# Optimization experiments

Hardware: AMD Instinct MI355X
Metric: run time of the kernel (lower is better)

The kernel has to match this reference:

```python
import math
import jax, jax.numpy as jnp
import numpy as np

L, D, H, F, V, S = 4, 1024, 16, 4096, 50257, 2048
HS = D // H
EPS = 1e-5
STD = 0.02


def setup_inputs() -> dict:
    key = jax.random.key(0)
    keys = iter(jax.random.split(key, 24))

    def rn(shape):
        return (jax.random.normal(next(keys), shape, jnp.float32) * STD)

    inp = {
        "input_ids": jax.random.randint(next(keys), (1, S), 0, V, dtype=jnp.int64),
        "tok_emb": rn((V, D)),
        "pos_emb": rn((S, D)),
        # per-layer stacked params; linear weights stored [in, out]
        "Wq": rn((L, D, D)), "bq": jnp.zeros((L, D)),
        "Wk": rn((L, D, D)), "bk": jnp.zeros((L, D)),
        "Wv": rn((L, D, D)), "bv": jnp.zeros((L, D)),
        "Wo": rn((L, D, D)), "bo": jnp.zeros((L, D)),
        "W1": rn((L, D, F)), "b1": jnp.zeros((L, F)),
        "W2": rn((L, F, D)), "b2": jnp.zeros((L, D)),
        "ln1w": jnp.ones((L, D)), "ln1b": jnp.zeros((L, D)),
        "ln2w": jnp.ones((L, D)), "ln2b": jnp.zeros((L, D)),
        "lnfw": jnp.ones((D,)), "lnfb": jnp.zeros((D,)),
        "lm_head": rn((V, D)),  # torch Linear weight layout [out, in]
    }
    return inp


def _layernorm(x, w, b):
    m = jnp.mean(x, axis=-1, keepdims=True)
    v = jnp.mean(jnp.square(x - m), axis=-1, keepdims=True)
    return (x - m) * jax.lax.rsqrt(v + EPS) * w + b


def reference(input_ids, tok_emb, pos_emb, Wq, bq, Wk, bk, Wv, bv, Wo, bo,
              W1, b1, W2, b2, ln1w, ln1b, ln2w, ln2b, lnfw, lnfb, lm_head):
    B, Sq = input_ids.shape
    h = tok_emb[input_ids] + pos_emb[None, :Sq]  # [B,S,D]
    causal = jnp.tril(jnp.ones((Sq, Sq), dtype=bool))
    scale = 1.0 / math.sqrt(HS)

    def block(h, p):
        wq, bq_, wk, bk_, wv, bv_, wo, bo_, w1, b1_, w2, b2_, l1w, l1b, l2w, l2b = p
        x = _layernorm(h, l1w, l1b)
        q = (x @ wq + bq_).reshape(B, Sq, H, HS).transpose(0, 2, 1, 3)
        k = (x @ wk + bk_).reshape(B, Sq, H, HS).transpose(0, 2, 1, 3)
        v = (x @ wv + bv_).reshape(B, Sq, H, HS).transpose(0, 2, 1, 3)
        scores = jnp.einsum('bhqd,bhkd->bhqk', q, k) * scale
        scores = jnp.where(causal, scores, jnp.finfo(scores.dtype).min)
        attn = jax.nn.softmax(scores, axis=-1)  # dropout is identity at eval
        out = jnp.einsum('bhqk,bhkd->bhqd', attn, v)
        out = out.transpose(0, 2, 1, 3).reshape(B, Sq, D)
        h = h + out @ wo + bo_
        x = _layernorm(h, l2w, l2b)
        h = h + jax.nn.gelu(x @ w1 + b1_, approximate=False) @ w2 + b2_
        return h, None

    h, _ = jax.lax.scan(block, h, (Wq, bq, Wk, bk, Wv, bv, Wo, bo,
                                   W1, b1, W2, b2, ln1w, ln1b, ln2w, ln2b))
    h = _layernorm(h, lnfw, lnfb)
    logits = h @ lm_head.T  # [B,S,V]
    return logits
```

## Files before the change

kernel.cpp:

```cpp
#include <hip/hip_runtime.h>
#include <math.h>
#include <stdint.h>


#define SEQ 2048
#define DIM 1024
#define NHEAD 16
#define FFN 4096
#define VOCAB 50257
#define NLAYER 4
#define LNEPS 1e-5f
#define QKVD 3072
#define KVB 128

using bf16x8 = __attribute__((ext_vector_type(8))) short;
using s16x4  = __attribute__((ext_vector_type(4))) short;
using f32x4  = __attribute__((ext_vector_type(4))) float;
using fl4    = __attribute__((ext_vector_type(4))) float;

static __device__ __forceinline__ short f2bf(float f) {
  uint32_t u = __float_as_uint(f);
  u = (u + 0x7fffu + ((u >> 16) & 1u)) >> 16;
  return (short)u;
}
static __device__ __forceinline__ float bf2f(short s) {
  return __uint_as_float(((uint32_t)(uint16_t)s) << 16);
}
static __device__ __forceinline__ void gload_lds16(const void* g, void* l) {
  __builtin_amdgcn_global_load_lds((const __attribute__((address_space(1))) void*)g,
                                   (__attribute__((address_space(3))) void*)l, 16, 0, 0);
}

__global__ void embed_kernel(const int* __restrict__ ids,
                             const float* __restrict__ tok,
                             const float* __restrict__ pos,
                             float* __restrict__ h) {
  int i = blockIdx.x * blockDim.x + threadIdx.x;
  if (i < SEQ * DIM) {
    int s = i / DIM, d = i % DIM;
    h[i] = tok[(long)ids[s] * DIM + d] + pos[i];
  }
}

__global__ void ln_kernel(const float* __restrict__ x, const float* __restrict__ w,
                          const float* __restrict__ b, short* __restrict__ y) {
  int row = blockIdx.x;
  const float* xr = x + (long)row * DIM;
  short* yr = y + (long)row * DIM;
  int tid = threadIdx.x;
  float v0 = xr[tid], v1 = xr[tid + 256], v2 = xr[tid + 512], v3 = xr[tid + 768];
  __shared__ float red[8];
  float s = v0 + v1 + v2 + v3;
#pragma unroll
  for (int o = 32; o >= 1; o >>= 1) s += __shfl_xor(s, o);
  if ((tid & 63) == 0) red[tid >> 6] = s;
  __syncthreads();
  float mean = (red[0] + red[1] + red[2] + red[3]) * (1.f / DIM);
  float d0 = v0 - mean, d1 = v1 - mean, d2 = v2 - mean, d3 = v3 - mean;
  float q = d0 * d0 + d1 * d1 + d2 * d2 + d3 * d3;
#pragma unroll
  for (int o = 32; o >= 1; o >>= 1) q += __shfl_xor(q, o);
  if ((tid & 63) == 0) red[4 + (tid >> 6)] = q;
  __syncthreads();
  float var = (red[4] + red[5] + red[6] + red[7]) * (1.f / DIM);
  float rstd = rsqrtf(var + LNEPS);
  yr[tid]       = f2bf(d0 * rstd * w[tid] + b[tid]);
  yr[tid + 256] = f2bf(d1 * rstd * w[tid + 256] + b[tid + 256]);
  yr[tid + 512] = f2bf(d2 * rstd * w[tid + 512] + b[tid + 512]);
  yr[tid + 768] = f2bf(d3 * rstd * w[tid + 768] + b[tid + 768]);
}

__global__ void transpose_w(const float* __restrict__ in, short* __restrict__ out,
                            int K, int N) {
  __shared__ float t[32][33];
  int c0 = blockIdx.x * 32, r0 = blockIdx.y * 32;
  int tx = threadIdx.x & 31, ty = threadIdx.x >> 5;
#pragma unroll
  for (int i = 0; i < 4; i++)
    t[ty + i * 8][tx] = in[(long)(r0 + ty + i * 8) * N + c0 + tx];
  __syncthreads();
#pragma unroll
  for (int i = 0; i < 4; i++)
    out[(long)(c0 + ty + i * 8) * K + r0 + tx] = f2bf(t[tx][ty + i * 8]);
}

struct TW4 { const float* src[4]; short* dst[4]; };
__global__ void transpose_w4(TW4 p) {
  const float* in = p.src[blockIdx.z];
  short* out = p.dst[blockIdx.z];
  __shared__ float t[32][33];
  int c0 = blockIdx.x * 32, r0 = blockIdx.y * 32;
  int tx = threadIdx.x & 31, ty = threadIdx.x >> 5;
#pragma unroll
  for (int i = 0; i < 4; i++)
    t[ty + i * 8][tx] = in[(long)(r0 + ty + i * 8) * DIM + c0 + tx];
  __syncthreads();
#pragma unroll
  for (int i = 0; i < 4; i++)
    out[(long)(c0 + ty + i * 8) * DIM + r0 + tx] = f2bf(t[tx][ty + i * 8]);
}

__global__ void transpose_v(const short* __restrict__ qkv, short* __restrict__ vt) {
  __shared__ short t[64][72];
  int s0 = blockIdx.x * 64, c0 = blockIdx.y * 64;
  int tid = threadIdx.x;
#pragma unroll
  for (int i = 0; i < 2; i++) {
    int ca = i * 256 + tid;
    int row = ca >> 3, cp = ca & 7;
    bf16x8 v = *(const bf16x8*)(qkv + (long)(s0 + row) * QKVD + 2 * DIM + c0 + cp * 8);
    *(bf16x8*)&t[row][cp * 8] = v;
  }
  __syncthreads();
#pragma unroll
  for (int i = 0; i < 2; i++) {
    int ca = i * 256 + tid;
    int crow = ca >> 3, sp = ca & 7;
    s16x4 a, b;
#pragma unroll
    for (int u = 0; u < 4; u++) a[u] = t[sp * 8 + u][crow];
#pragma unroll
    for (int u = 0; u < 4; u++) b[u] = t[sp * 8 + 4 + u][crow];
    bf16x8 o;
#pragma unroll
    for (int u = 0; u < 4; u++) { o[u] = a[u]; o[4 + u] = b[u]; }
    *(bf16x8*)(vt + (long)(c0 + crow) * SEQ + s0 + sp * 8) = o;
  }
}

__global__ void conv_bf16(const float* __restrict__ in, short* __restrict__ out, long n4) {
  long i = (long)blockIdx.x * blockDim.x + threadIdx.x;
  long stride = (long)gridDim.x * blockDim.x;
  for (; i < n4; i += stride) {
    fl4 v = *(const fl4*)(in + i * 4);
    s16x4 o;
    o[0] = f2bf(v[0]); o[1] = f2bf(v[1]); o[2] = f2bf(v[2]); o[3] = f2bf(v[3]);
    *(s16x4*)(out + i * 4) = o;
  }
}

__global__ void bias_cat(const float* __restrict__ bq, const float* __restrict__ bk,
                         const float* __restrict__ bv, float* __restrict__ out) {
  int i = blockIdx.x * 256 + threadIdx.x;
  if (i < QKVD) out[i] = i < DIM ? bq[i] : (i < 2 * DIM ? bk[i - DIM] : bv[i - 2 * DIM]);
}

template <bool GELU, bool RES, bool BIAS, bool OUTBF16, int KS, bool XCDSWZ>
__global__ __launch_bounds__(512) void gemm8(
    const short* __restrict__ A, const short* __restrict__ Bt,
    const float* __restrict__ bias, const float* __restrict__ res,
    void* __restrict__ Cout, int N, int Kfull) {
  __shared__ short lds[3][(256 + 128) * 64];
  const int tid = threadIdx.x, wid = tid >> 6, lane = tid & 63;
  const int l16 = lane & 15, lg = lane >> 4;
  int bx = blockIdx.x, by = blockIdx.y;
  if (XCDSWZ) {
    int gx = gridDim.x, nwg = gx * gridDim.y;
    int flat = by * gx + bx;
    int nf = (flat & 7) * (nwg >> 3) + (flat >> 3);
    bx = nf % gx; by = nf / gx;
  }
  const long m0 = (long)bx * 256, n0 = (long)by * 128;
  const int K = Kfull / KS;
  const int kbase = blockIdx.z * K;
  const int NT = K / 64;
  const int wr = (wid >> 1) * 64, wc = (wid & 1) * 64;

#define STAGE8(t, b)                                                            \
  {                                                                             \
    short* As_ = lds[b];                                                        \
    short* Bs_ = lds[b] + 256 * 64;                                             \
    int kk_ = kbase + (t) * 64;                                                 \
    _Pragma("unroll")                                                           \
    for (int i_ = 0; i_ < 4; i_++) {                                            \
      int ca_ = i_ * 512 + tid;                                                 \
      int row_ = ca_ >> 3, cp_ = ca_ & 7, c_ = cp_ ^ (row_ & 7);                \
      gload_lds16(A + (m0 + row_) * (long)Kfull + kk_ + c_ * 8,                 \
                  As_ + (i_ * 512 + wid * 64) * 8);                             \
    }                                                                           \
    _Pragma("unroll")                                                           \
    for (int i_ = 0; i_ < 2; i_++) {                                            \
      int ca_ = i_ * 512 + tid;                                                 \
      int row_ = ca_ >> 3, cp_ = ca_ & 7, c_ = cp_ ^ (row_ & 7);                \
      int rowb_ = (int)n0 + row_;                                               \
      if (rowb_ > N - 1) rowb_ = N - 1;                                         \
      gload_lds16(Bt + (long)rowb_ * Kfull + kk_ + c_ * 8,                      \
                  Bs_ + (i_ * 512 + wid * 64) * 8);                             \
    }                                                                           \
  }

  f32x4 acc[4][4] = {};
  STAGE8(0, 0);
  STAGE8(1, 1);
  asm volatile("s_waitcnt vmcnt(6)" ::: "memory");
  __builtin_amdgcn_s_barrier();
  __builtin_amdgcn_sched_barrier(0);

  for (int t = 0; t < NT; t++) {
    const int b = t % 3;
    if (t + 2 < NT) STAGE8(t + 2, (t + 2) % 3);
    const short* As = lds[b];
    const short* Bs = lds[b] + 256 * 64;
    bf16x8 af[4][2], bfr[4][2];
#pragma unroll
    for (int m = 0; m < 4; m++) {
      int row = wr + m * 16 + l16;
#pragma unroll
      for (int ks = 0; ks < 2; ks++)
        af[m][ks] = *(const bf16x8*)((const char*)As + row * 128 + (((ks * 4 + lg) ^ (row & 7)) * 16));
    }
#pragma unroll
    for (int n = 0; n < 4; n++) {
      int row = wc + n * 16 + l16;
#pragma unroll
      for (int ks = 0; ks < 2; ks++)
        bfr[n][ks] = *(const bf16x8*)((const char*)Bs + row * 128 + (((ks * 4 + lg) ^ (row & 7)) * 16));
    }
    __builtin_amdgcn_s_setprio(1);
#pragma unroll
    for (int ks = 0; ks < 2; ks++)
#pragma unroll
      for (int m = 0; m < 4; m++)
#pragma unroll
        for (int n = 0; n < 4; n++)
          acc[m][n] = __builtin_amdgcn_mfma_f32_16x16x32_bf16(af[m][ks], bfr[n][ks], acc[m][n], 0, 0, 0);
    __builtin_amdgcn_s_setprio(0);
    if (t + 2 < NT) {
      asm volatile("s_waitcnt vmcnt(6)" ::: "memory");
    } else if (t + 1 < NT) {
      asm volatile("s_waitcnt vmcnt(0)" ::: "memory");
    }
    if (t + 1 < NT) {
      __builtin_amdgcn_s_barrier();
      __builtin_amdgcn_sched_barrier(0);
    }
  }
#undef STAGE8

  const int lr4 = lg * 4;
  if (KS == 1) {
#pragma unroll
    for (int m = 0; m < 4; m++)
#pragma unroll
      for (int n = 0; n < 4; n++)
#pragma unroll
        for (int r = 0; r < 4; r++) {
          long row = m0 + wr + m * 16 + lr4 + r;
          long col = n0 + wc + n * 16 + l16;
          if (col < N) {
            float v = acc[m][n][r];
            if (BIAS) v += bias[col];
            if (GELU) v = 0.5f * v * (1.f + erff(v * 0.70710678118f));
            if (RES) v += res[row * (long)N + col];
            if (OUTBF16) ((short*)Cout)[row * (long)N + col] = f2bf(v);
            else ((float*)Cout)[row * (long)N + col] = v;
          }
        }
  } else {
    long M = (long)gridDim.x * 256;
    float* P = (float*)Cout + (long)blockIdx.z * M * N;
#pragma unroll
    for (int m = 0; m < 4; m++)
#pragma unroll
      for (int n = 0; n < 4; n++)
#pragma unroll
        for (int r = 0; r < 4; r++) {
          long row = m0 + wr + m * 16 + lr4 + r;
          long col = n0 + wc + n * 16 + l16;
          P[row * (long)N + col] = acc[m][n][r];
        }
  }
}

template <int KS>
__global__ void reduce_k(const float* __restrict__ part, const float* __restrict__ bias,
                         float* __restrict__ h, int N, long MN) {
  long i = ((long)blockIdx.x * 256 + threadIdx.x) * 4;
  if (i >= MN) return;
  fl4 s = *(const fl4*)(h + i);
  fl4 b = *(const fl4*)(bias + (int)(i % N));
  s[0] += b[0]; s[1] += b[1]; s[2] += b[2]; s[3] += b[3];
#pragma unroll
  for (int ks = 0; ks < KS; ks++) {
    fl4 p = *(const fl4*)(part + (long)ks * MN + i);
    s[0] += p[0]; s[1] += p[1]; s[2] += p[2]; s[3] += p[3];
  }
  *(fl4*)(h + i) = s;
}

__global__ __launch_bounds__(256) void attn_mfma(const short* __restrict__ qkv,
                                                 const short* __restrict__ vtg,
                                                 short* __restrict__ Oa) {
  int hh = blockIdx.x, qb = blockIdx.y;
  int q0 = qb * 64;
  int tid = threadIdx.x, wv = tid >> 6, lane = tid & 63;
  int l16 = lane & 15, lg = lane >> 4;
  int hcol = hh * 64;
  __shared__ short Ks[KVB * 64];
  __shared__ short Vt[64 * KVB];
  __shared__ short Pl[4][16 * KVB];

  bf16x8 qf[2];
  {
    const short* qrow = qkv + (long)(q0 + wv * 16 + l16) * QKVD + hcol;
#pragma unroll
    for (int dc = 0; dc < 2; dc++) {
      bf16x8 t = *(const bf16x8*)(qrow + dc * 32 + lg * 8);
#pragma unroll
      for (int j = 0; j < 8; j++) t[j] = f2bf(bf2f(t[j]) * 0.125f);
      qf[dc] = t;
    }
  }
  f32x4 of[4] = {};
  float mrun[4], lrun[4];
#pragma unroll
  for (int r = 0; r < 4; r++) { mrun[r] = -3e38f; lrun[r] = 0.f; }

  int nt = qb / 2 + 1;
  for (int kt = 0; kt < nt; kt++) {
    int k0 = kt * KVB;
    __syncthreads();
#pragma unroll
    for (int i = 0; i < 4; i++) {
      int ca = i * 256 + tid;
      int row = ca >> 3, cp = ca & 7, c = cp ^ (row & 7);
      int ldsoff = (i * 256 + wv * 64) * 8;
      gload_lds16(qkv + (long)(k0 + row) * QKVD + DIM + hcol + c * 8, (short*)Ks + ldsoff);
    }
#pragma unroll
    for (int i = 0; i < 4; i++) {
      int ca = i * 256 + tid;
      int row = ca >> 4, cp = ca & 15, c = cp ^ (row & 7);
      int ldsoff = (i * 256 + wv * 64) * 8;
      gload_lds16(vtg + (long)(hcol + row) * SEQ + k0 + c * 8, (short*)Vt + ldsoff);
    }
    __syncthreads();

    f32x4 sacc[8] = {};
#pragma unroll
    for (int kc = 0; kc < 8; kc++) {
      int row = kc * 16 + l16;
#pragma unroll
      for (int dc = 0; dc < 2; dc++) {
        bf16x8 kf = *(const bf16x8*)((const char*)Ks + row * 128 + (((dc * 4 + lg) ^ (row & 7)) * 16));
        sacc[kc] = __builtin_amdgcn_mfma_f32_16x16x32_bf16(qf[dc], kf, sacc[kc], 0, 0, 0);
      }
    }

    float sv[8][4], pf[8][4];
#pragma unroll
    for (int kc = 0; kc < 8; kc++)
#pragma unroll
      for (int r = 0; r < 4; r++) sv[kc][r] = sacc[kc][r];
    if (kt == nt - 1) {
#pragma unroll
      for (int kc = 0; kc < 8; kc++)
#pragma unroll
        for (int r = 0; r < 4; r++) {
          int kg = k0 + kc * 16 + l16;
          int rg = q0 + wv * 16 + lg * 4 + r;
          if (kg > rg) sv[kc][r] = -3e38f;
        }
    }
    float corr[4];
#pragma unroll
    for (int r = 0; r < 4; r++) {
      float m01 = fmaxf(sv[0][r], sv[1][r]), m23 = fmaxf(sv[2][r], sv[3][r]);
      float m45 = fmaxf(sv[4][r], sv[5][r]), m67 = fmaxf(sv[6][r], sv[7][r]);
      float mt = fmaxf(fmaxf(m01, m23), fmaxf(m45, m67));
#pragma unroll
      for (int o = 8; o >= 1; o >>= 1) mt = fmaxf(mt, __shfl_xor(mt, o));
      float mn = fmaxf(mrun[r], mt);
      corr[r] = __expf(mrun[r] - mn);
      mrun[r] = mn;
      float ps = 0.f;
#pragma unroll
      for (int kc = 0; kc < 8; kc++) {
        float p = __expf(sv[kc][r] - mn);
        pf[kc][r] = p;
        ps += p;
      }
#pragma unroll
      for (int o = 8; o >= 1; o >>= 1) ps += __shfl_xor(ps, o);
      lrun[r] = lrun[r] * corr[r] + ps;
    }
#pragma unroll
    for (int c = 0; c < 4; c++)
#pragma unroll
      for (int r = 0; r < 4; r++) of[c][r] *= corr[r];
#pragma unroll
    for (int kc = 0; kc < 8; kc++)
#pragma unroll
      for (int r = 0; r < 4; r++) {
        int row = lg * 4 + r, col = kc * 16 + l16;
        int chunk = col >> 3;
        *(short*)((char*)Pl[wv] + row * 256 + ((chunk ^ (row & 7)) * 16) + (col & 7) * 2) = f2bf(pf[kc][r]);
      }
    bf16x8 pfr[4];
#pragma unroll
    for (int kc2 = 0; kc2 < 4; kc2++) {
      int cl = kc2 * 4 + lg;
      pfr[kc2] = *(const bf16x8*)((const char*)Pl[wv] + l16 * 256 + ((cl ^ (l16 & 7)) * 16));
    }
#pragma unroll
    for (int c = 0; c < 4; c++)
#pragma unroll
      for (int kc2 = 0; kc2 < 4; kc2++) {
        int vrow = c * 16 + l16;
        int cl = kc2 * 4 + lg;
        bf16x8 vf = *(const bf16x8*)((const char*)Vt + vrow * 256 + ((cl ^ (vrow & 7)) * 16));
        of[c] = __builtin_amdgcn_mfma_f32_16x16x32_bf16(pfr[kc2], vf, of[c], 0, 0, 0);
      }
  }
#pragma unroll
  for (int c = 0; c < 4; c++)
#pragma unroll
    for (int r = 0; r < 4; r++) {
      int rowg = q0 + wv * 16 + lg * 4 + r;
      int colg = hcol + c * 16 + l16;
      Oa[(long)rowg * DIM + colg] = f2bf(of[c][r] / lrun[r]);
    }
}

extern "C" void kernel_launch(void* const* d_in, const int* in_sizes, int n_in,
                              void* d_out, int out_size, void* d_ws, size_t ws_size,
                              hipStream_t stream) {
  const int* ids = (const int*)d_in[0];
  const float* tok = (const float*)d_in[1];
  const float* pos = (const float*)d_in[2];
  const float* Wq = (const float*)d_in[3];
  const float* bq = (const float*)d_in[4];
  const float* Wk = (const float*)d_in[5];
  const float* bk = (const float*)d_in[6];
  const float* Wv = (const float*)d_in[7];
  const float* bv = (const float*)d_in[8];
  const float* Wo = (const float*)d_in[9];
  const float* bo = (const float*)d_in[10];
  const float* W1 = (const float*)d_in[11];
  const float* b1 = (const float*)d_in[12];
  const float* W2 = (const float*)d_in[13];
  const float* b2 = (const float*)d_in[14];
  const float* ln1w = (const float*)d_in[15];
  const float* ln1b = (const float*)d_in[16];
  const float* ln2w = (const float*)d_in[17];
  const float* ln2b = (const float*)d_in[18];
  const float* lnfw = (const float*)d_in[19];
  const float* lnfb = (const float*)d_in[20];
  const float* lmh = (const float*)d_in[21];
  float* out = (float*)d_out;

  char* wsb = (char*)d_ws;
  float* h = (float*)wsb;
  short* x = (short*)(wsb + 8388608);
  char* big = wsb + 8388608 + 4194304;
  short* qkv  = (short*)big;
  short* a    = (short*)(big + 12582912);
  short* vt   = (short*)(big + 16777216);
  short* fbuf = (short*)(big + 20971520);
  float* pproj = (float*)fbuf;
  float* pffn2 = (float*)big;
  char* wdyn = big + 37748736;
  short* wqkvT = (short*)wdyn;
  short* woT   = (short*)(wdyn + 6291456);
  short* w1T   = (short*)(wdyn + 8388608);
  short* w2T   = (short*)(wdyn + 16777216);
  float* bias3 = (float*)(wdyn + 25165824);
  short* lmhB = (short*)big;

  const long MN = (long)SEQ * DIM;

  embed_kernel<<<(SEQ * DIM + 255) / 256, 256, 0, stream>>>(ids, tok, pos, h);

  dim3 gQKV(SEQ / 256, QKVD / 128);
  dim3 gPROJ(SEQ / 256, DIM / 128, 2);
  dim3 gFFN1(SEQ / 256, FFN / 128);
  dim3 gFFN2(SEQ / 256, DIM / 128, 2);
  dim3 gV(SEQ / 256, (VOCAB + 127) / 128);

  for (int l = 0; l < NLAYER; l++) {
    TW4 tw;
    tw.src[0] = Wq + (long)l * DIM * DIM; tw.dst[0] = wqkvT;
    tw.src[1] = Wk + (long)l * DIM * DIM; tw.dst[1] = wqkvT + (long)DIM * DIM;
    tw.src[2] = Wv + (long)l * DIM * DIM; tw.dst[2] = wqkvT + (long)2 * DIM * DIM;
    tw.src[3] = Wo + (long)l * DIM * DIM; tw.dst[3] = woT;
    transpose_w4<<<dim3(32, 32, 4), 256, 0, stream>>>(tw);
    transpose_w<<<dim3(128, 32), 256, 0, stream>>>(W1 + (long)l * DIM * FFN, w1T, DIM, FFN);
    transpose_w<<<dim3(32, 128), 256, 0, stream>>>(W2 + (long)l * FFN * DIM, w2T, FFN, DIM);
    bias_cat<<<12, 256, 0, stream>>>(bq + (long)l * DIM, bk + (long)l * DIM, bv + (long)l * DIM, bias3);

    ln_kernel<<<SEQ, 256, 0, stream>>>(h, ln1w + (long)l * DIM, ln1b + (long)l * DIM, x);
    gemm8<false, false, true, true, 1, true><<<gQKV, 512, 0, stream>>>(x, wqkvT, bias3, nullptr, qkv, QKVD, DIM);
    transpose_v<<<dim3(SEQ / 64, DIM / 64), 256, 0, stream>>>(qkv, vt);
    attn_mfma<<<dim3(NHEAD, SEQ / 64), 256, 0, stream>>>(qkv, vt, a);
    gemm8<false, false, false, false, 2, true><<<gPROJ, 512, 0, stream>>>(a, woT, nullptr, nullptr, pproj, DIM, DIM);
    reduce_k<2><<<(int)(MN / 1024), 256, 0, stream>>>(pproj, bo + (long)l * DIM, h, DIM, MN);
    ln_kernel<<<SEQ, 256, 0, stream>>>(h, ln2w + (long)l * DIM, ln2b + (long)l * DIM, x);
    gemm8<true, false, true, true, 1, true><<<gFFN1, 512, 0, stream>>>(x, w1T, b1 + (long)l * FFN, nullptr, fbuf, FFN, DIM);
    gemm8<false, false, false, false, 2, true><<<gFFN2, 512, 0, stream>>>(fbuf, w2T, nullptr, nullptr, pffn2, DIM, FFN);
    reduce_k<2><<<(int)(MN / 1024), 256, 0, stream>>>(pffn2, b2 + (long)l * DIM, h, DIM, MN);
  }

  ln_kernel<<<SEQ, 256, 0, stream>>>(h, lnfw, lnfb, x);
  conv_bf16<<<2048, 256, 0, stream>>>(lmh, lmhB, (long)VOCAB * DIM / 4);
  gemm8<false, false, false, false, 1, true><<<gV, 512, 0, stream>>>(x, lmhB, nullptr, nullptr, out, VOCAB, DIM);
}
```

Before: 1.145 ms.

## Replace 256x128x64 GEMM tile with 128x128x32 tile, 4 waves, 3 blocks per CU

Swaps the 8-wave GEMM kernel (256x128 output tile, K-step 64) for a 4-wave version with a 128x128 tile and K-step 32, changing the LDS swizzle to match the 64-byte rows. The smaller LDS footprint and launch_bounds(256,3) let more workgroups share each CU, and grids double along M so more blocks are available for the many GEMMs. In exchange, each block reuses its data less, more K iterations with barriers are needed, and each sync covers fewer MFMAs.

```diff
diff --git a/kernel.cpp b/kernel.cpp
--- a/kernel.cpp
+++ b/kernel.cpp
@@ -146,11 +146,11 @@
 }
 
 template <bool GELU, bool RES, bool BIAS, bool OUTBF16, int KS, bool XCDSWZ>
-__global__ __launch_bounds__(512) void gemm8(
+__global__ __launch_bounds__(256, 3) void gemm4(
     const short* __restrict__ A, const short* __restrict__ Bt,
     const float* __restrict__ bias, const float* __restrict__ res,
     void* __restrict__ Cout, int N, int Kfull) {
-  __shared__ short lds[3][(256 + 128) * 64];
+  __shared__ short lds[3][(128 + 128) * 32];
   const int tid = threadIdx.x, wid = tid >> 6, lane = tid & 63;
   const int l16 = lane & 15, lg = lane >> 4;
   int bx = blockIdx.x, by = blockIdx.y;
@@ -160,73 +160,67 @@
     int nf = (flat & 7) * (nwg >> 3) + (flat >> 3);
     bx = nf % gx; by = nf / gx;
   }
-  const long m0 = (long)bx * 256, n0 = (long)by * 128;
+  const long m0 = (long)bx * 128, n0 = (long)by * 128;
   const int K = Kfull / KS;
   const int kbase = blockIdx.z * K;
-  const int NT = K / 64;
+  const int NT = K / 32;
   const int wr = (wid >> 1) * 64, wc = (wid & 1) * 64;
 
-#define STAGE8(t, b)                                                            \
+#define STAGE4(t, b)                                                            \
   {                                                                             \
     short* As_ = lds[b];                                                        \
-    short* Bs_ = lds[b] + 256 * 64;                                             \
-    int kk_ = kbase + (t) * 64;                                                 \
+    short* Bs_ = lds[b] + 128 * 32;                                             \
+    int kk_ = kbase + (t) * 32;                                                 \
     _Pragma("unroll")                                                           \
-    for (int i_ = 0; i_ < 4; i_++) {                                            \
-      int ca_ = i_ * 512 + tid;                                                 \
-      int row_ = ca_ >> 3, cp_ = ca_ & 7, c_ = cp_ ^ (row_ & 7);                \
+    for (int i_ = 0; i_ < 2; i_++) {                                            \
+      int ca_ = i_ * 256 + tid;                                                 \
+      int row_ = ca_ >> 2, cp_ = ca_ & 3, c_ = cp_ ^ ((row_ >> 1) & 3);         \
       gload_lds16(A + (m0 + row_) * (long)Kfull + kk_ + c_ * 8,                 \
-                  As_ + (i_ * 512 + wid * 64) * 8);                             \
+                  As_ + (i_ * 256 + wid * 64) * 8);                             \
     }                                                                           \
     _Pragma("unroll")                                                           \
     for (int i_ = 0; i_ < 2; i_++) {                                            \
-      int ca_ = i_ * 512 + tid;                                                 \
-      int row_ = ca_ >> 3, cp_ = ca_ & 7, c_ = cp_ ^ (row_ & 7);                \
+      int ca_ = i_ * 256 + tid;                                                 \
+      int row_ = ca_ >> 2, cp_ = ca_ & 3, c_ = cp_ ^ ((row_ >> 1) & 3);         \
       int rowb_ = (int)n0 + row_;                                               \
       if (rowb_ > N - 1) rowb_ = N - 1;                                         \
       gload_lds16(Bt + (long)rowb_ * Kfull + kk_ + c_ * 8,                      \
-                  Bs_ + (i_ * 512 + wid * 64) * 8);                             \
+                  Bs_ + (i_ * 256 + wid * 64) * 8);                             \
     }                                                                           \
   }
 
   f32x4 acc[4][4] = {};
-  STAGE8(0, 0);
-  STAGE8(1, 1);
-  asm volatile("s_waitcnt vmcnt(6)" ::: "memory");
+  STAGE4(0, 0);
+  STAGE4(1, 1);
+  asm volatile("s_waitcnt vmcnt(4)" ::: "memory");
   __builtin_amdgcn_s_barrier();
   __builtin_amdgcn_sched_barrier(0);
 
   for (int t = 0; t < NT; t++) {
     const int b = t % 3;
-    if (t + 2 < NT) STAGE8(t + 2, (t + 2) % 3);
+    if (t + 2 < NT) STAGE4(t + 2, (t + 2) % 3);
     const short* As = lds[b];
-    const short* Bs = lds[b] + 256 * 64;
-    bf16x8 af[4][2], bfr[4][2];
+    const short* Bs = lds[b] + 128 * 32;
+    bf16x8 af[4], bfr[4];
 #pragma unroll
     for (int m = 0; m < 4; m++) {
       int row = wr + m * 16 + l16;
-#pragma unroll
-      for (int ks = 0; ks < 2; ks++)
-        af[m][ks] = *(const bf16x8*)((const char*)As + row * 128 + (((ks * 4 + lg) ^ (row & 7)) * 16));
+      af[m] = *(const bf16x8*)((const char*)As + row * 64 + ((lg ^ ((row >> 1) & 3)) * 16));
     }
 #pragma unroll
     for (int n = 0; n < 4; n++) {
       int row = wc + n * 16 + l16;
-#pragma unroll
-      for (int ks = 0; ks < 2; ks++)
-        bfr[n][ks] = *(const bf16x8*)((const char*)Bs + row * 128 + (((ks * 4 + lg) ^ (row & 7)) * 16));
+      bfr[n] = *(const bf16x8*)((const char*)Bs + row * 64 + ((lg ^ ((row >> 1) & 3)) * 16));
     }
     __builtin_amdgcn_s_setprio(1);
 #pragma unroll
-    for (int ks = 0; ks < 2; ks++)
-#pragma unroll
-      for (int m = 0; m < 4; m++)
-#pragma unroll
-        for (int n = 0; n < 4; n++)
-          acc[m][n] = __builtin_amdgcn_mfma_f32_16x16x32_bf16(af[m][ks], bfr[n][ks], acc[m][n], 0, 0, 0);
+    for (int m = 0; m < 4; m++)
+#pragma unroll
+      for (int n = 0; n < 4; n++)
+        acc[m][n] = __builtin_amdgcn_mfma_f32_16x16x32_bf16(af[m], bfr[n], acc[m][n], 0, 0, 0);
     __builtin_amdgcn_s_setprio(0);
     if (t + 2 < NT) {
-      asm volatile("s_waitcnt vmcnt(6)" ::: "memory");
+      asm volatile("s_waitcnt vmcnt(4)" ::: "memory");
     } else if (t + 1 < NT) {
       asm volatile("s_waitcnt vmcnt(0)" ::: "memory");
     }
@@ -235,7 +229,7 @@
       __builtin_amdgcn_sched_barrier(0);
     }
   }
-#undef STAGE8
+#undef STAGE4
 
   const int lr4 = lg * 4;
   if (KS == 1) {
@@ -257,7 +251,7 @@
           }
         }
   } else {
-    long M = (long)gridDim.x * 256;
+    long M = (long)gridDim.x * 128;
     float* P = (float*)Cout + (long)blockIdx.z * M * N;
 #pragma unroll
     for (int m = 0; m < 4; m++)
@@ -471,11 +465,11 @@
 
   embed_kernel<<<(SEQ * DIM + 255) / 256, 256, 0, stream>>>(ids, tok, pos, h);
 
-  dim3 gQKV(SEQ / 256, QKVD / 128);
-  dim3 gPROJ(SEQ / 256, DIM / 128, 2);
-  dim3 gFFN1(SEQ / 256, FFN / 128);
-  dim3 gFFN2(SEQ / 256, DIM / 128, 2);
-  dim3 gV(SEQ / 256, (VOCAB + 127) / 128);
+  dim3 gQKV(SEQ / 128, QKVD / 128);
+  dim3 gPROJ(SEQ / 128, DIM / 128, 2);
+  dim3 gFFN1(SEQ / 128, FFN / 128);
+  dim3 gFFN2(SEQ / 128, DIM / 128, 2);
+  dim3 gV(SEQ / 128, (VOCAB + 127) / 128);
 
   for (int l = 0; l < NLAYER; l++) {
     TW4 tw;
@@ -489,18 +483,18 @@
     bias_cat<<<12, 256, 0, stream>>>(bq + (long)l * DIM, bk + (long)l * DIM, bv + (long)l * DIM, bias3);
 
     ln_kernel<<<SEQ, 256, 0, stream>>>(h, ln1w + (long)l * DIM, ln1b + (long)l * DIM, x);
-    gemm8<false, false, true, true, 1, true><<<gQKV, 512, 0, stream>>>(x, wqkvT, bias3, nullptr, qkv, QKVD, DIM);
+    gemm4<false, false, true, true, 1, true><<<gQKV, 256, 0, stream>>>(x, wqkvT, bias3, nullptr, qkv, QKVD, DIM);
     transpose_v<<<dim3(SEQ / 64, DIM / 64), 256, 0, stream>>>(qkv, vt);
     attn_mfma<<<dim3(NHEAD, SEQ / 64), 256, 0, stream>>>(qkv, vt, a);
-    gemm8<false, false, false, false, 2, true><<<gPROJ, 512, 0, stream>>>(a, woT, nullptr, nullptr, pproj, DIM, DIM);
+    gemm4<false, false, false, false, 2, true><<<gPROJ, 256, 0, stream>>>(a, woT, nullptr, nullptr, pproj, DIM, DIM);
     reduce_k<2><<<(int)(MN / 1024), 256, 0, stream>>>(pproj, bo + (long)l * DIM, h, DIM, MN);
     ln_kernel<<<SEQ, 256, 0, stream>>>(h, ln2w + (long)l * DIM, ln2b + (long)l * DIM, x);
-    gemm8<true, false, true, true, 1, true><<<gFFN1, 512, 0, stream>>>(x, w1T, b1 + (long)l * FFN, nullptr, fbuf, FFN, DIM);
-    gemm8<false, false, false, false, 2, true><<<gFFN2, 512, 0, stream>>>(fbuf, w2T, nullptr, nullptr, pffn2, DIM, FFN);
+    gemm4<true, false, true, true, 1, true><<<gFFN1, 256, 0, stream>>>(x, w1T, b1 + (long)l * FFN, nullptr, fbuf, FFN, DIM);
+    gemm4<false, false, false, false, 2, true><<<gFFN2, 256, 0, stream>>>(fbuf, w2T, nullptr, nullptr, pffn2, DIM, FFN);
     reduce_k<2><<<(int)(MN / 1024), 256, 0, stream>>>(pffn2, b2 + (long)l * DIM, h, DIM, MN);
   }
 
   ln_kernel<<<SEQ, 256, 0, stream>>>(h, lnfw, lnfb, x);
   conv_bf16<<<2048, 256, 0, stream>>>(lmh, lmhB, (long)VOCAB * DIM / 4);
-  gemm8<false, false, false, false, 1, true><<<gV, 512, 0, stream>>>(x, lmhB, nullptr, nullptr, out, VOCAB, DIM);
-}
+  gemm4<false, false, false, false, 1, true><<<gV, 256, 0, stream>>>(x, lmhB, nullptr, nullptr, out, VOCAB, DIM);
+}
```

Measured after the change: 1.151 ms. No clear change (+0.6%).
